# Optimization experiments

Hardware: AMD Instinct MI355X
Metric: run time of the kernel (lower is better)

Reference implementation:

```python
import jax, jax.numpy as jnp
import numpy as np

N = 50000          # nodes
E = 800000         # edges
F_IN = 128         # num_node_features
H = 64             # hidden_channels
G = 64             # graphs in batch
C = 10             # num_classes
L_HID = 3          # num_hidden_layers
EPS = 1e-5


def setup_inputs() -> dict:
    key = jax.random.key(0)
    ks = jax.random.split(key, 16)
    x = jax.random.normal(ks[0], (N, F_IN), dtype=jnp.float32)
    edge_index = jax.random.randint(ks[1], (2, E), 0, N, dtype=jnp.int32)
    batch = jnp.sort(jax.random.randint(ks[2], (N,), 0, G, dtype=jnp.int32))
    s = 0.05
    W_in = jax.random.normal(ks[3], (F_IN, H), dtype=jnp.float32) * s
    b_in = jnp.zeros((H,), dtype=jnp.float32)
    W_hid = jax.random.normal(ks[4], (L_HID, H, H), dtype=jnp.float32) * s
    b_hid = jnp.zeros((L_HID, H), dtype=jnp.float32)
    gamma = jnp.ones((H,), dtype=jnp.float32)
    beta = jnp.zeros((H,), dtype=jnp.float32)
    # MLPReadout: 64 -> 32 -> 16 -> 10
    W1 = jax.random.normal(ks[5], (H, H // 2), dtype=jnp.float32) * s
    b1 = jnp.zeros((H // 2,), dtype=jnp.float32)
    W2 = jax.random.normal(ks[6], (H // 2, H // 4), dtype=jnp.float32) * s
    b2 = jnp.zeros((H // 4,), dtype=jnp.float32)
    W3 = jax.random.normal(ks[7], (H // 4, C), dtype=jnp.float32) * s
    b3 = jnp.zeros((C,), dtype=jnp.float32)
    return {"x": x, "edge_index": edge_index, "batch": batch,
            "W_in": W_in, "b_in": b_in, "W_hid": W_hid, "b_hid": b_hid,
            "gamma": gamma, "beta": beta,
            "W1": W1, "b1": b1, "W2": W2, "b2": b2, "W3": W3, "b3": b3}


def gcn_conv(h_pre, W, b, src, dst, dis):
    # PyG GCNConv with self-loops: out_i = sum_{j->i} d_i^-.5 d_j^-.5 (x_j W) + d_i^-1 (x_i W) + b
    h = h_pre @ W                                   # [N, H]
    norm = (dis[src] * dis[dst])[:, None]           # [E, 1]
    agg = jax.ops.segment_sum(h[src] * norm, dst, num_segments=N)
    agg = agg + h * (dis * dis)[:, None]            # self-loop term
    return agg + b


def batchnorm(x, gamma, beta):
    mu = jnp.mean(x, axis=0)
    var = jnp.mean(jnp.square(x - mu), axis=0)      # biased var (torch BN)
    return (x - mu) * jax.lax.rsqrt(var + EPS) * gamma + beta


def reference(x, edge_index, batch, W_in, b_in, W_hid, b_hid,
              gamma, beta, W1, b1, W2, b2, W3, b3):
    src, dst = edge_index[0], edge_index[1]
    # degree with self-loops (computed on target nodes)
    deg = jax.ops.segment_sum(jnp.ones((E,), x.dtype), dst, num_segments=N) + 1.0
    dis = jax.lax.rsqrt(deg)                        # deg^-0.5

    h = jax.nn.relu(gcn_conv(x, W_in, b_in, src, dst, dis))
    for l in range(L_HID):
        h = gcn_conv(h, W_hid[l], b_hid[l], src, dst, dis)
        h = batchnorm(h, gamma, beta)
        h = jax.nn.relu(h)

    # global mean pool over graphs
    sums = jax.ops.segment_sum(h, batch, num_segments=G)           # [G, H]
    cnts = jax.ops.segment_sum(jnp.ones((N,), x.dtype), batch, num_segments=G)
    pooled = sums / jnp.maximum(cnts, 1.0)[:, None]

    # MLPReadout
    y = jax.nn.relu(pooled @ W1 + b1)
    y = jax.nn.relu(y @ W2 + b2)
    return y @ W3 + b3                               # [G, C]
```

## Files before the change

kernel.cpp:

```cpp
#include <hip/hip_runtime.h>

#define NN 50000
#define NE 800000
#define FIN 128
#define H 64
#define NG 64
#define NC 10
#define EPS 1e-5f
#define NB_SCAN 196
#define GATHER_BLOCKS 12500
#define BNRED_BLOCKS 125

__global__ void count_deg_kernel(const int* __restrict__ dst, int* __restrict__ deg) {
    int e = blockIdx.x * blockDim.x + threadIdx.x;
    if (e < NE) atomicAdd(&deg[dst[e]], 1);
}

__global__ void make_dis_kernel(const int* __restrict__ deg, float* __restrict__ dis) {
    int i = blockIdx.x * blockDim.x + threadIdx.x;
    if (i < NN) dis[i] = rsqrtf((float)deg[i] + 1.0f);
}

__global__ void scan1_kernel(const int* __restrict__ deg, int* __restrict__ ebase,
                             int* __restrict__ bsum) {
    __shared__ int s[256];
    int t = threadIdx.x;
    int i = blockIdx.x * 256 + t;
    int v = (i < NN) ? deg[i] : 0;
    s[t] = v;
    for (int off = 1; off < 256; off <<= 1) {
        __syncthreads();
        int add = (t >= off) ? s[t - off] : 0;
        __syncthreads();
        s[t] += add;
    }
    __syncthreads();
    if (i < NN) ebase[i] = s[t] - v;
    if (t == 255) bsum[blockIdx.x] = s[255];
}

__global__ void scan2_kernel(int* __restrict__ bsum) {
    __shared__ int s[256];
    int t = threadIdx.x;
    int v = (t < NB_SCAN) ? bsum[t] : 0;
    s[t] = v;
    for (int off = 1; off < 256; off <<= 1) {
        __syncthreads();
        int add = (t >= off) ? s[t - off] : 0;
        __syncthreads();
        s[t] += add;
    }
    __syncthreads();
    if (t < NB_SCAN) bsum[t] = s[t] - v;
}

__global__ void scan3_kernel(int* __restrict__ ebase, const int* __restrict__ bsum) {
    int i = blockIdx.x * blockDim.x + threadIdx.x;
    if (i < NN) ebase[i] += bsum[i >> 8];
    if (i == 0) ebase[NN] = NE;
}

__global__ void fill_kernel(const int* __restrict__ src, const int* __restrict__ dst,
                            const int* __restrict__ ebase, int* __restrict__ cursor,
                            const float* __restrict__ dis, int* __restrict__ eidx,
                            float* __restrict__ enorm) {
    int e = blockIdx.x * blockDim.x + threadIdx.x;
    if (e < NE) {
        int s = src[e], d = dst[e];
        int slot = ebase[d] + atomicAdd(&cursor[d], 1);
        eidx[slot] = s;
        enorm[slot] = dis[s] * dis[d];
    }
}

__global__ __launch_bounds__(256, 4) void gemm_fin_kernel(const float* __restrict__ A,
                                                          const float* __restrict__ W,
                                                          float* __restrict__ outp) {
    __shared__ float Al[64][65];
    __shared__ float Wl[64 * H];
    const int tid = threadIdx.x;
    const int r0 = blockIdx.x * 64;
    const int row = tid >> 2;
    const int cb  = (tid & 3) << 4;
    float acc[16];
#pragma unroll
    for (int j = 0; j < 16; j++) acc[j] = 0.f;

    for (int k0 = 0; k0 < FIN; k0 += 64) {
        for (int idx = tid; idx < 64 * H; idx += 256) Wl[idx] = W[k0 * H + idx];
        for (int idx = tid; idx < 64 * 64; idx += 256) {
            int r = idx >> 6, c = idx & 63;
            int gr = r0 + r;
            Al[r][c] = (gr < NN) ? A[(long)gr * FIN + k0 + c] : 0.f;
        }
        __syncthreads();
#pragma unroll
        for (int k = 0; k < 64; k++) {
            float a = Al[row][k];
#pragma unroll
            for (int j = 0; j < 16; j++) acc[j] = fmaf(a, Wl[k * H + cb + j], acc[j]);
        }
        __syncthreads();
    }
    int gr = r0 + row;
    if (gr < NN) {
        float4* o = reinterpret_cast<float4*>(&outp[(long)gr * H + cb]);
        o[0] = make_float4(acc[0], acc[1], acc[2], acc[3]);
        o[1] = make_float4(acc[4], acc[5], acc[6], acc[7]);
        o[2] = make_float4(acc[8], acc[9], acc[10], acc[11]);
        o[3] = make_float4(acc[12], acc[13], acc[14], acc[15]);
    }
}

template <int DO_BN>
__global__ __launch_bounds__(256, 4) void gemm_hid_kernel(const float* __restrict__ A,
                                                          const float* __restrict__ W,
                                                          const float* __restrict__ bnsc,
                                                          float* __restrict__ outp) {
    __shared__ float Al[64][65];
    __shared__ float Wl[64 * H];
    __shared__ float bns[128];
    const int tid = threadIdx.x;
    if (DO_BN && tid < 128) bns[tid] = bnsc[tid];
    const int r0 = blockIdx.x * 64;
    const int row = tid >> 2;
    const int cb  = (tid & 3) << 4;
    float acc[16];
#pragma unroll
    for (int j = 0; j < 16; j++) acc[j] = 0.f;

    if (DO_BN) __syncthreads();
    for (int idx = tid; idx < 64 * H; idx += 256) Wl[idx] = W[idx];
    for (int idx = tid; idx < 64 * 64; idx += 256) {
        int r = idx >> 6, c = idx & 63;
        int gr = r0 + r;
        float a = (gr < NN) ? A[(long)gr * H + c] : 0.f;
        if (DO_BN) a = fmaxf(fmaf(a, bns[c], bns[64 + c]), 0.f);
        Al[r][c] = a;
    }
    __syncthreads();
#pragma unroll
    for (int k = 0; k < 64; k++) {
        float a = Al[row][k];
#pragma unroll
        for (int j = 0; j < 16; j++) acc[j] = fmaf(a, Wl[k * H + cb + j], acc[j]);
    }
    int gr = r0 + row;
    if (gr < NN) {
        float4* o = reinterpret_cast<float4*>(&outp[(long)gr * H + cb]);
        o[0] = make_float4(acc[0], acc[1], acc[2], acc[3]);
        o[1] = make_float4(acc[4], acc[5], acc[6], acc[7]);
        o[2] = make_float4(acc[8], acc[9], acc[10], acc[11]);
        o[3] = make_float4(acc[12], acc[13], acc[14], acc[15]);
    }
}

template <int MODE>
__global__ __launch_bounds__(256) void gather_kernel(const float* __restrict__ hw,
                                                     const int* __restrict__ ebase,
                                                     const int* __restrict__ eidx,
                                                     const float* __restrict__ enorm,
                                                     const float* __restrict__ dis,
                                                     const float* __restrict__ bias,
                                                     float* __restrict__ outp,
                                                     float* __restrict__ pbn) {
    __shared__ float ls[H], lss[H];
    if (MODE == 1) {
        if (threadIdx.x < H) { ls[threadIdx.x] = 0.f; lss[threadIdx.x] = 0.f; }
        __syncthreads();
    }
    const int node = blockIdx.x * 4 + (threadIdx.x >> 6);
    const int lane = threadIdx.x & 63;
    const int grp  = lane >> 4;
    const int c4   = (lane & 15) << 2;
    const int e0 = ebase[node], e1 = ebase[node + 1];
    float4 acc = make_float4(0.f, 0.f, 0.f, 0.f);
    for (int e = e0 + grp; e < e1; e += 4) {
        float nrm = enorm[e];
        const float4 v = *reinterpret_cast<const float4*>(&hw[(long)eidx[e] * H + c4]);
        acc.x = fmaf(v.x, nrm, acc.x);
        acc.y = fmaf(v.y, nrm, acc.y);
        acc.z = fmaf(v.z, nrm, acc.z);
        acc.w = fmaf(v.w, nrm, acc.w);
    }
#pragma unroll
    for (int m = 16; m <= 32; m <<= 1) {
        acc.x += __shfl_xor(acc.x, m, 64);
        acc.y += __shfl_xor(acc.y, m, 64);
        acc.z += __shfl_xor(acc.z, m, 64);
        acc.w += __shfl_xor(acc.w, m, 64);
    }
    float ds = dis[node];
    float d2 = ds * ds;
    const float4 self = *reinterpret_cast<const float4*>(&hw[(long)node * H + c4]);
    float4 v;
    v.x = fmaf(self.x, d2, acc.x) + bias[c4 + 0];
    v.y = fmaf(self.y, d2, acc.y) + bias[c4 + 1];
    v.z = fmaf(self.z, d2, acc.z) + bias[c4 + 2];
    v.w = fmaf(self.w, d2, acc.w) + bias[c4 + 3];
    if (MODE == 0) {
        v.x = fmaxf(v.x, 0.f); v.y = fmaxf(v.y, 0.f);
        v.z = fmaxf(v.z, 0.f); v.w = fmaxf(v.w, 0.f);
    }
    if (grp == 0) {
        *reinterpret_cast<float4*>(&outp[(long)node * H + c4]) = v;
        if (MODE == 1) {
            atomicAdd(&ls[c4 + 0], v.x); atomicAdd(&lss[c4 + 0], v.x * v.x);
            atomicAdd(&ls[c4 + 1], v.y); atomicAdd(&lss[c4 + 1], v.y * v.y);
            atomicAdd(&ls[c4 + 2], v.z); atomicAdd(&lss[c4 + 2], v.z * v.z);
            atomicAdd(&ls[c4 + 3], v.w); atomicAdd(&lss[c4 + 3], v.w * v.w);
        }
    }
    if (MODE == 1) {
        __syncthreads();
        if (threadIdx.x < H) {
            pbn[(long)blockIdx.x * 128 + threadIdx.x] = ls[threadIdx.x];
            pbn[(long)blockIdx.x * 128 + H + threadIdx.x] = lss[threadIdx.x];
        }
    }
}

__global__ void bnredA_kernel(const float* __restrict__ pbn, float* __restrict__ pbn2) {
    int c = threadIdx.x & 127;
    int half = threadIdx.x >> 7;
    int r0 = blockIdx.x * 100;
    float s = 0.f;
    for (int r = r0 + half; r < r0 + 100; r += 2) s += pbn[(long)r * 128 + c];
    __shared__ float red[256];
    red[threadIdx.x] = s;
    __syncthreads();
    if (half == 0) pbn2[(long)blockIdx.x * 128 + c] = red[c] + red[128 + c];
}

__global__ void bnredB_kernel(const float* __restrict__ pbn2, const float* __restrict__ gamma,
                              const float* __restrict__ beta, float* __restrict__ bnsc) {
    int t = threadIdx.x;
    int c = t & 127;
    int half = t >> 7;
    float s = 0.f;
    for (int r = half; r < BNRED_BLOCKS; r += 2) s += pbn2[(long)r * 128 + c];
    __shared__ float red[256];
    __shared__ float tot[128];
    red[t] = s;
    __syncthreads();
    if (t < 128) tot[t] = red[t] + red[128 + t];
    __syncthreads();
    if (t < H) {
        float mu  = tot[t] * (1.0f / NN);
        float var = tot[H + t] * (1.0f / NN) - mu * mu;
        float sc  = rsqrtf(var + EPS) * gamma[t];
        bnsc[t]     = sc;
        bnsc[H + t] = beta[t] - mu * sc;
    }
}

__global__ void gstart_kernel(const int* __restrict__ batch, int* __restrict__ gstart) {
    int g = threadIdx.x;
    if (g <= NG) {
        int lo = 0, hi = NN;
        while (lo < hi) {
            int mid = (lo + hi) >> 1;
            if (batch[mid] < g) lo = mid + 1; else hi = mid;
        }
        gstart[g] = lo;
    }
}

__global__ void pool_bn_kernel(const float* __restrict__ conv, const float* __restrict__ bnsc,
                               const int* __restrict__ gstart, float* __restrict__ pooled) {
    int g = blockIdx.x;
    int n0 = gstart[g], n1 = gstart[g + 1];
    int sub = threadIdx.x >> 6, lane = threadIdx.x & 63;
    float sc = bnsc[lane], sh = bnsc[H + lane];
    float s = 0.f;
    for (int n = n0 + sub; n < n1; n += 4)
        s += fmaxf(fmaf(conv[(long)n * H + lane], sc, sh), 0.f);
    __shared__ float red[256];
    red[threadIdx.x] = s;
    __syncthreads();
    if (sub == 0) {
        float tot = red[lane] + red[64 + lane] + red[128 + lane] + red[192 + lane];
        float inv = 1.0f / fmaxf((float)(n1 - n0), 1.0f);
        pooled[g * H + lane] = tot * inv;
    }
}

__global__ void mlp_kernel(const float* __restrict__ pooled,
                           const float* __restrict__ W1, const float* __restrict__ b1,
                           const float* __restrict__ W2, const float* __restrict__ b2,
                           const float* __restrict__ W3, const float* __restrict__ b3,
                           float* __restrict__ out) {
    __shared__ float pl[H], y1[32], y2[16];
    int g = blockIdx.x, t = threadIdx.x;
    pl[t] = pooled[g * H + t];
    __syncthreads();
    if (t < 32) {
        float s = b1[t];
        for (int k = 0; k < H; k++) s += pl[k] * W1[k * 32 + t];
        y1[t] = fmaxf(s, 0.f);
    }
    __syncthreads();
    if (t < 16) {
        float s = b2[t];
        for (int k = 0; k < 32; k++) s += y1[k] * W2[k * 16 + t];
        y2[t] = fmaxf(s, 0.f);
    }
    __syncthreads();
    if (t < NC) {
        float s = b3[t];
        for (int k = 0; k < 16; k++) s += y2[k] * W3[k * NC + t];
        out[g * NC + t] = s;
    }
}

extern "C" void kernel_launch(void* const* d_in, const int* in_sizes, int n_in,
                              void* d_out, int out_size, void* d_ws, size_t ws_size,
                              hipStream_t stream) {
    const float* x     = (const float*)d_in[0];
    const int*   ei    = (const int*)d_in[1];
    const int*   batch = (const int*)d_in[2];
    const float* W_in  = (const float*)d_in[3];
    const float* b_in  = (const float*)d_in[4];
    const float* W_hid = (const float*)d_in[5];
    const float* b_hid = (const float*)d_in[6];
    const float* gamma = (const float*)d_in[7];
    const float* beta  = (const float*)d_in[8];
    const float* W1    = (const float*)d_in[9];
    const float* b1    = (const float*)d_in[10];
    const float* W2    = (const float*)d_in[11];
    const float* b2    = (const float*)d_in[12];
    const float* W3    = (const float*)d_in[13];
    const float* b3    = (const float*)d_in[14];
    float* out = (float*)d_out;

    const int* src = ei;
    const int* dst = ei + NE;

    int*   deg_i  = (int*)d_ws;
    int*   ebase  = deg_i + 50048;
    int*   cursor = ebase + 50056;
    int*   eidx   = cursor + 50048;
    int*   bsum   = eidx + 800000;
    int*   gstart = bsum + 256;
    float* dis    = (float*)(gstart + 72);
    float* enorm  = dis + 50048;
    float* hw     = enorm + 800000;
    float* conv   = hw + (long)NN * H;
    float* h      = conv + (long)NN * H;
    float* pbn    = h + (long)NN * H;
    float* pbn2   = pbn + (long)GATHER_BLOCKS * 128;
    float* bnsc   = pbn2 + BNRED_BLOCKS * 128;
    float* pooled = bnsc + 128;

    const int NB_GEMM = (NN + 63) / 64;
    const int NB_E    = (NE + 255) / 256;
    const int NB_N    = (NN + 255) / 256;

    hipMemsetAsync(deg_i, 0, 50048 * sizeof(int), stream);
    hipMemsetAsync(cursor, 0, 50048 * sizeof(int), stream);
    count_deg_kernel<<<NB_E, 256, 0, stream>>>(dst, deg_i);
    make_dis_kernel<<<NB_N, 256, 0, stream>>>(deg_i, dis);
    scan1_kernel<<<NB_SCAN, 256, 0, stream>>>(deg_i, ebase, bsum);
    scan2_kernel<<<1, 256, 0, stream>>>(bsum);
    scan3_kernel<<<NB_N, 256, 0, stream>>>(ebase, bsum);
    fill_kernel<<<NB_E, 256, 0, stream>>>(src, dst, ebase, cursor, dis, eidx, enorm);
    gstart_kernel<<<1, 128, 0, stream>>>(batch, gstart);

    gemm_fin_kernel<<<NB_GEMM, 256, 0, stream>>>(x, W_in, hw);
    gather_kernel<0><<<GATHER_BLOCKS, 256, 0, stream>>>(hw, ebase, eidx, enorm, dis, b_in, h, nullptr);

    for (int l = 0; l < 3; l++) {
        if (l == 0)
            gemm_hid_kernel<0><<<NB_GEMM, 256, 0, stream>>>(h, W_hid, nullptr, hw);
        else
            gemm_hid_kernel<1><<<NB_GEMM, 256, 0, stream>>>(conv, W_hid + (long)l * H * H, bnsc, hw);
        gather_kernel<1><<<GATHER_BLOCKS, 256, 0, stream>>>(hw, ebase, eidx, enorm, dis,
                                                            b_hid + (long)l * H, conv, pbn);
        bnredA_kernel<<<BNRED_BLOCKS, 256, 0, stream>>>(pbn, pbn2);
        bnredB_kernel<<<1, 256, 0, stream>>>(pbn2, gamma, beta, bnsc);
    }

    pool_bn_kernel<<<NG, 256, 0, stream>>>(conv, bnsc, gstart, pooled);
    mlp_kernel<<<NG, H, 0, stream>>>(pooled, W1, b1, W2, b2, W3, b3, out);
}
```

Baseline: 661.4 us.

## Fold symmetric GCN normalization into GEMM epilogue and fuse small kernels

```diff
diff --git a/kernel.cpp b/kernel.cpp
--- a/kernel.cpp
+++ b/kernel.cpp
@@ -16,17 +16,13 @@
     if (e < NE) atomicAdd(&deg[dst[e]], 1);
 }
 
-__global__ void make_dis_kernel(const int* __restrict__ deg, float* __restrict__ dis) {
-    int i = blockIdx.x * blockDim.x + threadIdx.x;
-    if (i < NN) dis[i] = rsqrtf((float)deg[i] + 1.0f);
-}
-
 __global__ void scan1_kernel(const int* __restrict__ deg, int* __restrict__ ebase,
-                             int* __restrict__ bsum) {
+                             int* __restrict__ bsum, float* __restrict__ dis) {
     __shared__ int s[256];
     int t = threadIdx.x;
     int i = blockIdx.x * 256 + t;
     int v = (i < NN) ? deg[i] : 0;
+    if (i < NN) dis[i] = rsqrtf((float)v + 1.0f);
     s[t] = v;
     for (int off = 1; off < 256; off <<= 1) {
         __syncthreads();
@@ -39,9 +35,18 @@
     if (t == 255) bsum[blockIdx.x] = s[255];
 }
 
-__global__ void scan2_kernel(int* __restrict__ bsum) {
+__global__ void scan2_kernel(int* __restrict__ bsum, const int* __restrict__ batch,
+                             int* __restrict__ gstart) {
+    int t = threadIdx.x;
+    if (t <= NG) {
+        int lo = 0, hi = NN;
+        while (lo < hi) {
+            int mid = (lo + hi) >> 1;
+            if (batch[mid] < t) lo = mid + 1; else hi = mid;
+        }
+        gstart[t] = lo;
+    }
     __shared__ int s[256];
-    int t = threadIdx.x;
     int v = (t < NB_SCAN) ? bsum[t] : 0;
     s[t] = v;
     for (int off = 1; off < 256; off <<= 1) {
@@ -62,19 +67,18 @@
 
 __global__ void fill_kernel(const int* __restrict__ src, const int* __restrict__ dst,
                             const int* __restrict__ ebase, int* __restrict__ cursor,
-                            const float* __restrict__ dis, int* __restrict__ eidx,
-                            float* __restrict__ enorm) {
+                            int* __restrict__ eidx) {
     int e = blockIdx.x * blockDim.x + threadIdx.x;
     if (e < NE) {
-        int s = src[e], d = dst[e];
+        int d = dst[e];
         int slot = ebase[d] + atomicAdd(&cursor[d], 1);
-        eidx[slot] = s;
-        enorm[slot] = dis[s] * dis[d];
+        eidx[slot] = src[e];
     }
 }
 
 __global__ __launch_bounds__(256, 4) void gemm_fin_kernel(const float* __restrict__ A,
                                                           const float* __restrict__ W,
+                                                          const float* __restrict__ dis,
                                                           float* __restrict__ outp) {
     __shared__ float Al[64][65];
     __shared__ float Wl[64 * H];
@@ -104,6 +108,9 @@
     }
     int gr = r0 + row;
     if (gr < NN) {
+        float ds = dis[gr];
+#pragma unroll
+        for (int j = 0; j < 16; j++) acc[j] *= ds;
         float4* o = reinterpret_cast<float4*>(&outp[(long)gr * H + cb]);
         o[0] = make_float4(acc[0], acc[1], acc[2], acc[3]);
         o[1] = make_float4(acc[4], acc[5], acc[6], acc[7]);
@@ -115,13 +122,32 @@
 template <int DO_BN>
 __global__ __launch_bounds__(256, 4) void gemm_hid_kernel(const float* __restrict__ A,
                                                           const float* __restrict__ W,
-                                                          const float* __restrict__ bnsc,
+                                                          const float* __restrict__ pbn2,
+                                                          const float* __restrict__ gamma,
+                                                          const float* __restrict__ beta,
+                                                          const float* __restrict__ dis,
                                                           float* __restrict__ outp) {
     __shared__ float Al[64][65];
     __shared__ float Wl[64 * H];
     __shared__ float bns[128];
+    __shared__ float tot[128];
     const int tid = threadIdx.x;
-    if (DO_BN && tid < 128) bns[tid] = bnsc[tid];
+    if (DO_BN) {
+        if (tid < 128) {
+            float s = 0.f;
+            for (int r = 0; r < BNRED_BLOCKS; ++r) s += pbn2[(long)r * 128 + tid];
+            tot[tid] = s;
+        }
+        __syncthreads();
+        if (tid < H) {
+            float mu  = tot[tid] * (1.0f / NN);
+            float var = tot[H + tid] * (1.0f / NN) - mu * mu;
+            float sc  = rsqrtf(var + EPS) * gamma[tid];
+            bns[tid]     = sc;
+            bns[H + tid] = beta[tid] - mu * sc;
+        }
+        __syncthreads();
+    }
     const int r0 = blockIdx.x * 64;
     const int row = tid >> 2;
     const int cb  = (tid & 3) << 4;
@@ -129,7 +155,6 @@
 #pragma unroll
     for (int j = 0; j < 16; j++) acc[j] = 0.f;
 
-    if (DO_BN) __syncthreads();
     for (int idx = tid; idx < 64 * H; idx += 256) Wl[idx] = W[idx];
     for (int idx = tid; idx < 64 * 64; idx += 256) {
         int r = idx >> 6, c = idx & 63;
@@ -147,6 +172,9 @@
     }
     int gr = r0 + row;
     if (gr < NN) {
+        float ds = dis[gr];
+#pragma unroll
+        for (int j = 0; j < 16; j++) acc[j] *= ds;
         float4* o = reinterpret_cast<float4*>(&outp[(long)gr * H + cb]);
         o[0] = make_float4(acc[0], acc[1], acc[2], acc[3]);
         o[1] = make_float4(acc[4], acc[5], acc[6], acc[7]);
@@ -159,7 +187,6 @@
 __global__ __launch_bounds__(256) void gather_kernel(const float* __restrict__ hw,
                                                      const int* __restrict__ ebase,
                                                      const int* __restrict__ eidx,
-                                                     const float* __restrict__ enorm,
                                                      const float* __restrict__ dis,
                                                      const float* __restrict__ bias,
                                                      float* __restrict__ outp,
@@ -175,13 +202,19 @@
     const int c4   = (lane & 15) << 2;
     const int e0 = ebase[node], e1 = ebase[node + 1];
     float4 acc = make_float4(0.f, 0.f, 0.f, 0.f);
-    for (int e = e0 + grp; e < e1; e += 4) {
-        float nrm = enorm[e];
-        const float4 v = *reinterpret_cast<const float4*>(&hw[(long)eidx[e] * H + c4]);
-        acc.x = fmaf(v.x, nrm, acc.x);
-        acc.y = fmaf(v.y, nrm, acc.y);
-        acc.z = fmaf(v.z, nrm, acc.z);
-        acc.w = fmaf(v.w, nrm, acc.w);
+    int e = e0 + grp;
+    for (; e + 4 < e1; e += 8) {
+        int s0 = eidx[e], s1 = eidx[e + 4];
+        const float4 v0 = *reinterpret_cast<const float4*>(&hw[(long)s0 * H + c4]);
+        const float4 v1 = *reinterpret_cast<const float4*>(&hw[(long)s1 * H + c4]);
+        acc.x += v0.x + v1.x;
+        acc.y += v0.y + v1.y;
+        acc.z += v0.z + v1.z;
+        acc.w += v0.w + v1.w;
+    }
+    if (e < e1) {
+        const float4 v0 = *reinterpret_cast<const float4*>(&hw[(long)eidx[e] * H + c4]);
+        acc.x += v0.x; acc.y += v0.y; acc.z += v0.z; acc.w += v0.w;
     }
 #pragma unroll
     for (int m = 16; m <= 32; m <<= 1) {
@@ -190,14 +223,13 @@
         acc.z += __shfl_xor(acc.z, m, 64);
         acc.w += __shfl_xor(acc.w, m, 64);
     }
+    const float4 self = *reinterpret_cast<const float4*>(&hw[(long)node * H + c4]);
     float ds = dis[node];
-    float d2 = ds * ds;
-    const float4 self = *reinterpret_cast<const float4*>(&hw[(long)node * H + c4]);
     float4 v;
-    v.x = fmaf(self.x, d2, acc.x) + bias[c4 + 0];
-    v.y = fmaf(self.y, d2, acc.y) + bias[c4 + 1];
-    v.z = fmaf(self.z, d2, acc.z) + bias[c4 + 2];
-    v.w = fmaf(self.w, d2, acc.w) + bias[c4 + 3];
+    v.x = fmaf(acc.x + self.x, ds, bias[c4 + 0]);
+    v.y = fmaf(acc.y + self.y, ds, bias[c4 + 1]);
+    v.z = fmaf(acc.z + self.z, ds, bias[c4 + 2]);
+    v.w = fmaf(acc.w + self.w, ds, bias[c4 + 3]);
     if (MODE == 0) {
         v.x = fmaxf(v.x, 0.f); v.y = fmaxf(v.y, 0.f);
         v.z = fmaxf(v.z, 0.f); v.w = fmaxf(v.w, 0.f);
@@ -232,84 +264,62 @@
     if (half == 0) pbn2[(long)blockIdx.x * 128 + c] = red[c] + red[128 + c];
 }
 
-__global__ void bnredB_kernel(const float* __restrict__ pbn2, const float* __restrict__ gamma,
-                              const float* __restrict__ beta, float* __restrict__ bnsc) {
-    int t = threadIdx.x;
-    int c = t & 127;
-    int half = t >> 7;
-    float s = 0.f;
-    for (int r = half; r < BNRED_BLOCKS; r += 2) s += pbn2[(long)r * 128 + c];
+__global__ void pool_mlp_kernel(const float* __restrict__ conv, const float* __restrict__ pbn2,
+                                const float* __restrict__ gamma, const float* __restrict__ beta,
+                                const int* __restrict__ gstart,
+                                const float* __restrict__ W1, const float* __restrict__ b1,
+                                const float* __restrict__ W2, const float* __restrict__ b2,
+                                const float* __restrict__ W3, const float* __restrict__ b3,
+                                float* __restrict__ out) {
+    __shared__ float tot[128];
+    __shared__ float bns[128];
     __shared__ float red[256];
-    __shared__ float tot[128];
-    red[t] = s;
-    __syncthreads();
-    if (t < 128) tot[t] = red[t] + red[128 + t];
+    __shared__ float pl[H], y1[32], y2[16];
+    const int t = threadIdx.x;
+    const int g = blockIdx.x;
+    if (t < 128) {
+        float s = 0.f;
+        for (int r = 0; r < BNRED_BLOCKS; ++r) s += pbn2[(long)r * 128 + t];
+        tot[t] = s;
+    }
     __syncthreads();
     if (t < H) {
         float mu  = tot[t] * (1.0f / NN);
         float var = tot[H + t] * (1.0f / NN) - mu * mu;
         float sc  = rsqrtf(var + EPS) * gamma[t];
-        bnsc[t]     = sc;
-        bnsc[H + t] = beta[t] - mu * sc;
-    }
-}
-
-__global__ void gstart_kernel(const int* __restrict__ batch, int* __restrict__ gstart) {
-    int g = threadIdx.x;
-    if (g <= NG) {
-        int lo = 0, hi = NN;
-        while (lo < hi) {
-            int mid = (lo + hi) >> 1;
-            if (batch[mid] < g) lo = mid + 1; else hi = mid;
-        }
-        gstart[g] = lo;
-    }
-}
-
-__global__ void pool_bn_kernel(const float* __restrict__ conv, const float* __restrict__ bnsc,
-                               const int* __restrict__ gstart, float* __restrict__ pooled) {
-    int g = blockIdx.x;
-    int n0 = gstart[g], n1 = gstart[g + 1];
-    int sub = threadIdx.x >> 6, lane = threadIdx.x & 63;
-    float sc = bnsc[lane], sh = bnsc[H + lane];
+        bns[t]     = sc;
+        bns[H + t] = beta[t] - mu * sc;
+    }
+    __syncthreads();
+    const int n0 = gstart[g], n1 = gstart[g + 1];
+    const int sub = t >> 6, lane = t & 63;
+    float sc = bns[lane], sh = bns[H + lane];
     float s = 0.f;
     for (int n = n0 + sub; n < n1; n += 4)
         s += fmaxf(fmaf(conv[(long)n * H + lane], sc, sh), 0.f);
-    __shared__ float red[256];
-    red[threadIdx.x] = s;
+    red[t] = s;
     __syncthreads();
     if (sub == 0) {
-        float tot = red[lane] + red[64 + lane] + red[128 + lane] + red[192 + lane];
         float inv = 1.0f / fmaxf((float)(n1 - n0), 1.0f);
-        pooled[g * H + lane] = tot * inv;
-    }
-}
-
-__global__ void mlp_kernel(const float* __restrict__ pooled,
-                           const float* __restrict__ W1, const float* __restrict__ b1,
-                           const float* __restrict__ W2, const float* __restrict__ b2,
-                           const float* __restrict__ W3, const float* __restrict__ b3,
-                           float* __restrict__ out) {
-    __shared__ float pl[H], y1[32], y2[16];
-    int g = blockIdx.x, t = threadIdx.x;
-    pl[t] = pooled[g * H + t];
+        pl[lane] = (red[lane] + red[64 + lane] + red[128 + lane] + red[192 + lane]) * inv;
+    }
     __syncthreads();
     if (t < 32) {
-        float s = b1[t];
-        for (int k = 0; k < H; k++) s += pl[k] * W1[k * 32 + t];
-        y1[t] = fmaxf(s, 0.f);
+        float v = b1[t];
+        for (int k = 0; k < H; k++) v = fmaf(pl[k], W1[k * 32 + t], v);
+        y1[t] = fmaxf(v, 0.f);
     }
     __syncthreads();
     if (t < 16) {
-        float s = b2[t];
-        for (int k = 0; k < 32; k++) s += y1[k] * W2[k * 16 + t];
-        y2[t] = fmaxf(s, 0.f);
+        float v = b2[t];
+        for (int k = 0; k < 32; k++) v = fmaf(y1[k], W2[k * 16 + t], v);
+        y2[t] = fmaxf(v, 0.f);
     }
     __syncthreads();
     if (t < NC) {
-        float s = b3[t];
-        for (int k = 0; k < 16; k++) s += y2[k] * W3[k * NC + t];
-        out[g * NC + t] = s;
+        float v = b3[t];
+        for (int k = 0; k < 16; k++) v = fmaf(y2[k], W3[k * NC + t], v);
+        out[(long)g * NC + t] = v;
     }
 }
 
@@ -337,49 +347,43 @@
     const int* dst = ei + NE;
 
     int*   deg_i  = (int*)d_ws;
-    int*   ebase  = deg_i + 50048;
-    int*   cursor = ebase + 50056;
-    int*   eidx   = cursor + 50048;
+    int*   cursor = deg_i + 50048;
+    int*   ebase  = cursor + 50048;
+    int*   eidx   = ebase + 50056;
     int*   bsum   = eidx + 800000;
     int*   gstart = bsum + 256;
     float* dis    = (float*)(gstart + 72);
-    float* enorm  = dis + 50048;
-    float* hw     = enorm + 800000;
+    float* hw     = dis + 50048;
     float* conv   = hw + (long)NN * H;
     float* h      = conv + (long)NN * H;
     float* pbn    = h + (long)NN * H;
     float* pbn2   = pbn + (long)GATHER_BLOCKS * 128;
-    float* bnsc   = pbn2 + BNRED_BLOCKS * 128;
-    float* pooled = bnsc + 128;
 
     const int NB_GEMM = (NN + 63) / 64;
     const int NB_E    = (NE + 255) / 256;
     const int NB_N    = (NN + 255) / 256;
 
-    hipMemsetAsync(deg_i, 0, 50048 * sizeof(int), stream);
-    hipMemsetAsync(cursor, 0, 50048 * sizeof(int), stream);
+    hipMemsetAsync(deg_i, 0, 2 * 50048 * sizeof(int), stream);
     count_deg_kernel<<<NB_E, 256, 0, stream>>>(dst, deg_i);
-    make_dis_kernel<<<NB_N, 256, 0, stream>>>(deg_i, dis);
-    scan1_kernel<<<NB_SCAN, 256, 0, stream>>>(deg_i, ebase, bsum);
-    scan2_kernel<<<1, 256, 0, stream>>>(bsum);
+    scan1_kernel<<<NB_SCAN, 256, 0, stream>>>(deg_i, ebase, bsum, dis);
+    scan2_kernel<<<1, 256, 0, stream>>>(bsum, batch, gstart);
     scan3_kernel<<<NB_N, 256, 0, stream>>>(ebase, bsum);
-    fill_kernel<<<NB_E, 256, 0, stream>>>(src, dst, ebase, cursor, dis, eidx, enorm);
-    gstart_kernel<<<1, 128, 0, stream>>>(batch, gstart);
-
-    gemm_fin_kernel<<<NB_GEMM, 256, 0, stream>>>(x, W_in, hw);
-    gather_kernel<0><<<GATHER_BLOCKS, 256, 0, stream>>>(hw, ebase, eidx, enorm, dis, b_in, h, nullptr);
-
-    for (int l = 0; l < 3; l++) {
-        if (l == 0)
-            gemm_hid_kernel<0><<<NB_GEMM, 256, 0, stream>>>(h, W_hid, nullptr, hw);
-        else
-            gemm_hid_kernel<1><<<NB_GEMM, 256, 0, stream>>>(conv, W_hid + (long)l * H * H, bnsc, hw);
-        gather_kernel<1><<<GATHER_BLOCKS, 256, 0, stream>>>(hw, ebase, eidx, enorm, dis,
+    fill_kernel<<<NB_E, 256, 0, stream>>>(src, dst, ebase, cursor, eidx);
+
+    gemm_fin_kernel<<<NB_GEMM, 256, 0, stream>>>(x, W_in, dis, hw);
+    gather_kernel<0><<<GATHER_BLOCKS, 256, 0, stream>>>(hw, ebase, eidx, dis, b_in, h, nullptr);
+
+    gemm_hid_kernel<0><<<NB_GEMM, 256, 0, stream>>>(h, W_hid, nullptr, nullptr, nullptr, dis, hw);
+    gather_kernel<1><<<GATHER_BLOCKS, 256, 0, stream>>>(hw, ebase, eidx, dis, b_hid, conv, pbn);
+    bnredA_kernel<<<BNRED_BLOCKS, 256, 0, stream>>>(pbn, pbn2);
+    for (int l = 1; l < 3; l++) {
+        gemm_hid_kernel<1><<<NB_GEMM, 256, 0, stream>>>(conv, W_hid + (long)l * H * H, pbn2,
+                                                        gamma, beta, dis, hw);
+        gather_kernel<1><<<GATHER_BLOCKS, 256, 0, stream>>>(hw, ebase, eidx, dis,
                                                             b_hid + (long)l * H, conv, pbn);
         bnredA_kernel<<<BNRED_BLOCKS, 256, 0, stream>>>(pbn, pbn2);
-        bnredB_kernel<<<1, 256, 0, stream>>>(pbn2, gamma, beta, bnsc);
-    }
-
-    pool_bn_kernel<<<NG, 256, 0, stream>>>(conv, bnsc, gstart, pooled);
-    mlp_kernel<<<NG, H, 0, stream>>>(pooled, W1, b1, W2, b2, W3, b3, out);
-}
+    }
+
+    pool_mlp_kernel<<<NG, 256, 0, stream>>>(conv, pbn2, gamma, beta, gstart,
+                                            W1, b1, W2, b2, W3, b3, out);
+}
```

After: 609.7 us. -7.8%, faster.
